# Kernel optimization log

Measured on AMD Instinct MI355X. Metric: run time of the kernel, lower is better.

The kernel has to match this reference:

```python
import jax, jax.numpy as jnp
import numpy as np

B, T, OBS, S, OUT, H = 128, 2048, 128, 128, 64, 64
SCALE = 0.05  # keep the linear recurrence numerically stable over T steps


def setup_inputs() -> dict:
    key = jax.random.key(0)
    ks = jax.random.split(key, 8)
    return {
        "obs": jax.random.normal(ks[0], (B, T, OBS), dtype=jnp.float32),
        "x0": jnp.zeros((B, S), dtype=jnp.float32),
        "A_T": SCALE * jax.random.normal(ks[1], (S, S), dtype=jnp.float32),
        "By_T": SCALE * jax.random.normal(ks[2], (OBS, S), dtype=jnp.float32),
        "Cu_T": SCALE * jax.random.normal(ks[3], (S, OUT), dtype=jnp.float32),
        "Duy_T": SCALE * jax.random.normal(ks[4], (OBS, OUT), dtype=jnp.float32),
        "log_stds": jnp.full((OUT,), -1.6094379124341003, dtype=jnp.float32),
        "W0": SCALE * jax.random.normal(ks[5], (H, OBS), dtype=jnp.float32),
        "b0": jnp.zeros((H,), dtype=jnp.float32),
        "W1": SCALE * jax.random.normal(ks[6], (H, H), dtype=jnp.float32),
        "b1": jnp.zeros((H,), dtype=jnp.float32),
        "W2": SCALE * jax.random.normal(ks[7], (1, H), dtype=jnp.float32),
        "b2": jnp.zeros((1,), dtype=jnp.float32),
        "dt": jnp.float32(0.01),
    }


def reference(obs, x0, A_T, By_T, Cu_T, Duy_T, log_stds, W0, b0, W1, b1, W2, b2, dt):
    def xdot(x, y):
        return x @ A_T + y @ By_T

    def step(x, y):
        # control output at current state, then RK4 integration of x' = A x + B y
        u = x @ Cu_T + y @ Duy_T                      # [B, OUT]
        k1 = xdot(x, y)
        k2 = xdot(x + dt * k1 / 2, y)
        k3 = xdot(x + dt * k2 / 2, y)
        k4 = xdot(x + dt * k3, y)
        x_next = x + dt / 6 * (k1 + 2 * k2 + 2 * k3 + k4)
        return x_next, u

    obs_t = jnp.swapaxes(obs, 0, 1)                   # [T, B, OBS]
    x_final, actions_t = jax.lax.scan(step, x0, obs_t)
    actions = jnp.swapaxes(actions_t, 0, 1)           # [B, T, OUT]

    logs = jnp.broadcast_to(log_stds, (actions.shape[0], actions.shape[1], log_stds.shape[0]))
    outputs = jnp.concatenate([actions, logs], axis=2)  # [B, T, 2*OUT]

    # value MLP: Linear -> tanh -> Linear -> tanh -> Linear
    h = jnp.tanh(obs @ W0.T + b0)
    h = jnp.tanh(h @ W1.T + b1)
    cur_value = (h @ W2.T + b2).reshape(-1)           # [B*T]

    return outputs, cur_value, x_final
```

## Files before the change

### kernel.cpp

```cpp
#include <hip/hip_runtime.h>

#define B_    128
#define T_    2048
#define OBS_  128
#define S_    128
#define OUT_  64
#define H_    64
#define NR    (B_*T_)
#define K_CH  32
#define C_CH  64
#define VOFF  (NR*2*OUT_)
#define XFOFF (VOFF + NR)

typedef __attribute__((ext_vector_type(8))) short short8v;
typedef __attribute__((ext_vector_type(4))) float f32x4;

__device__ __forceinline__ unsigned short f2bf(float f){
  unsigned int u = __float_as_uint(f);
  u += 0x7FFFu + ((u >> 16) & 1u);
  return (unsigned short)(u >> 16);
}
__device__ __forceinline__ float bf2f(unsigned short h){
  return __uint_as_float(((unsigned int)h) << 16);
}

__global__ __launch_bounds__(256) void k_mm(const float* __restrict__ A,
                                            const float* __restrict__ B,
                                            float* __restrict__ C, int ldc){
  int e = blockIdx.x * 256 + threadIdx.x;
  int r = e >> 7, c = e & 127;
  float acc = 0.f;
  #pragma unroll 4
  for (int k = 0; k < 128; ++k) acc += A[r*128 + k] * B[k*128 + c];
  C[r*ldc + c] = acc;
}

__global__ __launch_bounds__(256) void k_build(const float* __restrict__ A_T,
                                               const float* __restrict__ A2,
                                               const float* __restrict__ A3,
                                               const float* __restrict__ A4,
                                               const float* __restrict__ Cu_T,
                                               const float* __restrict__ Duy_T,
                                               const float* __restrict__ dtp,
                                               float* __restrict__ M,
                                               unsigned short* __restrict__ Mmibf,
                                               float* __restrict__ P, float* __restrict__ Wcat,
                                               unsigned short* __restrict__ cubf){
  float dt = *dtp;
  float d2 = dt*dt*0.5f;
  float d3 = d2*dt*(1.f/3.f);
  float d4 = d3*dt*0.25f;
  int e = blockIdx.x * 256 + threadIdx.x;
  int r = e >> 7, c = e & 127;
  float eye = (r == c) ? 1.f : 0.f;
  float mi = dt*A_T[e] + d2*A2[e] + d3*A3[e] + d4*A4[e];
  M[e] = eye + mi;
  Mmibf[e] = f2bf(mi);
  P[e] = dt*eye + d2*A_T[e] + d3*A2[e] + d4*A3[e];
  if (e < 128*64){
    int k = e >> 6, o = e & 63;
    Wcat[k*192 + 128 + o] = Duy_T[e];
    cubf[e] = f2bf(Cu_T[e]);
  }
}

__global__ __launch_bounds__(256) void k_cvtw(const float* __restrict__ Wcat,
                                              const float* __restrict__ W0,
                                              const float* __restrict__ W1,
                                              unsigned short* __restrict__ Wbf,
                                              unsigned short* __restrict__ W0bf,
                                              unsigned short* __restrict__ W1bf){
  int e = blockIdx.x * 256 + threadIdx.x;
  if (e < 24576)       Wbf[e]          = f2bf(Wcat[e]);
  else if (e < 32768)  W0bf[e - 24576] = f2bf(W0[e - 24576]);
  else                 W1bf[e - 32768] = f2bf(W1[e - 32768]);
}

__global__ __launch_bounds__(256) void k_fused(const float* __restrict__ obs,
                                               const unsigned short* __restrict__ Wbf,
                                               const unsigned short* __restrict__ W0bf,
                                               const unsigned short* __restrict__ W1bf,
                                               const float* __restrict__ W2,
                                               const float* __restrict__ b0g,
                                               const float* __restrict__ b1g,
                                               const float* __restrict__ b2g,
                                               const float* __restrict__ ls,
                                               unsigned short* __restrict__ cuy,
                                               float* __restrict__ out){
  __shared__ __align__(16) unsigned short ct[128*200];
  __shared__ __align__(16) unsigned short h0l[128*80];
  __shared__ float pl[128][4];
  int tid = threadIdx.x;
  int lane = tid & 63, w = tid >> 6;
  size_t row0 = (size_t)blockIdx.x * 128;
  int colbase = w * 48;
  int colh    = w * 16;
  int lr = lane & 15;
  int lk = (lane >> 4) * 8;

  short8v bfrag[3][4];
  #pragma unroll
  for (int cf = 0; cf < 3; ++cf)
    #pragma unroll
    for (int kk = 0; kk < 4; ++kk){
      short8v b;
      #pragma unroll
      for (int j = 0; j < 8; ++j)
        b[j] = (short)Wbf[(size_t)(kk*32 + lk + j)*192 + (colbase + cf*16 + lr)];
      bfrag[cf][kk] = b;
    }
  short8v bw0[4];
  #pragma unroll
  for (int kk = 0; kk < 4; ++kk)
    bw0[kk] = *(const short8v*)&W0bf[(size_t)(colh + lr)*128 + kk*32 + lk];
  short8v bw1[2];
  #pragma unroll
  for (int kk = 0; kk < 2; ++kk)
    bw1[kk] = *(const short8v*)&W1bf[(size_t)(colh + lr)*64 + kk*32 + lk];
  float b0v = b0g[colh + lr];
  float b1v = b1g[colh + lr];
  float w2v = W2[colh + lr];

  for (int rf = 0; rf < 8; ++rf){
    f32x4 acc0 = {0.f,0.f,0.f,0.f}, acc1 = {0.f,0.f,0.f,0.f}, acc2 = {0.f,0.f,0.f,0.f};
    f32x4 acch = {0.f,0.f,0.f,0.f};
    const float* arow = obs + (row0 + (size_t)(rf*16 + lr)) * 128;
    #pragma unroll
    for (int kk = 0; kk < 4; ++kk){
      float4 a0 = *(const float4*)&arow[kk*32 + lk];
      float4 a1 = *(const float4*)&arow[kk*32 + lk + 4];
      short8v af;
      af[0] = (short)f2bf(a0.x); af[1] = (short)f2bf(a0.y);
      af[2] = (short)f2bf(a0.z); af[3] = (short)f2bf(a0.w);
      af[4] = (short)f2bf(a1.x); af[5] = (short)f2bf(a1.y);
      af[6] = (short)f2bf(a1.z); af[7] = (short)f2bf(a1.w);
      acc0 = __builtin_amdgcn_mfma_f32_16x16x32_bf16(af, bfrag[0][kk], acc0, 0, 0, 0);
      acc1 = __builtin_amdgcn_mfma_f32_16x16x32_bf16(af, bfrag[1][kk], acc1, 0, 0, 0);
      acc2 = __builtin_amdgcn_mfma_f32_16x16x32_bf16(af, bfrag[2][kk], acc2, 0, 0, 0);
      acch = __builtin_amdgcn_mfma_f32_16x16x32_bf16(af, bw0[kk],     acch, 0, 0, 0);
    }
    int orow = rf*16 + (lane >> 4)*4;
    #pragma unroll
    for (int j = 0; j < 4; ++j){
      ct[(orow + j)*200 + colbase      + lr] = f2bf(acc0[j]);
      ct[(orow + j)*200 + colbase + 16 + lr] = f2bf(acc1[j]);
      ct[(orow + j)*200 + colbase + 32 + lr] = f2bf(acc2[j]);
      h0l[(orow + j)*80 + colh + lr]         = f2bf(tanhf(acch[j] + b0v));
    }
  }
  __syncthreads();

  for (int li = tid; li < 128*24; li += 256){
    int r = li / 24, seg = li % 24;
    *(uint4*)&cuy[(row0 + r)*192 + seg*8] = *(const uint4*)&ct[r*200 + seg*8];
  }

  for (int rf = 0; rf < 8; ++rf){
    f32x4 acc = {b1v, b1v, b1v, b1v};
    #pragma unroll
    for (int kk = 0; kk < 2; ++kk){
      short8v af = *(const short8v*)&h0l[(rf*16 + lr)*80 + kk*32 + lk];
      acc = __builtin_amdgcn_mfma_f32_16x16x32_bf16(af, bw1[kk], acc, 0, 0, 0);
    }
    float4 vpart;
    #pragma unroll
    for (int j = 0; j < 4; ++j) (&vpart.x)[j] = tanhf(acc[j]) * w2v;
    #pragma unroll
    for (int m = 1; m < 16; m <<= 1){
      vpart.x += __shfl_xor(vpart.x, m);
      vpart.y += __shfl_xor(vpart.y, m);
      vpart.z += __shfl_xor(vpart.z, m);
      vpart.w += __shfl_xor(vpart.w, m);
    }
    if (lr == 0){
      int orow = rf*16 + (lane >> 4)*4;
      #pragma unroll
      for (int j = 0; j < 4; ++j) pl[orow + j][w] = (&vpart.x)[j];
    }
  }
  __syncthreads();

  if (tid < 128)
    out[(size_t)VOFF + row0 + tid] = pl[tid][0] + pl[tid][1] + pl[tid][2] + pl[tid][3] + b2g[0];
  for (int li = tid; li < 128*16; li += 256){
    int r = li >> 4, c4 = li & 15;
    float4 lv = *(const float4*)&ls[c4*4];
    *(float4*)&out[(row0 + r)*128 + 64 + c4*4] = lv;
  }
}

__global__ __launch_bounds__(256) void k_phase1(const unsigned short* __restrict__ cuy,
                                                const unsigned short* __restrict__ Mmibf,
                                                float* __restrict__ Dd){
  __shared__ __align__(16) unsigned short xw[32*136];
  int tid = threadIdx.x;
  int lane = tid & 63, w = tid >> 6;
  int lr = lane & 15, lg = lane >> 4;
  int ci = blockIdx.x >> 2, bi = blockIdx.x & 3;
  int b0 = bi*32, t0 = ci*K_CH;
  int colbase = w*32;

  short8v bm[2][4];
  #pragma unroll
  for (int ctt = 0; ctt < 2; ++ctt)
    #pragma unroll
    for (int kk = 0; kk < 4; ++kk){
      short8v b;
      #pragma unroll
      for (int j = 0; j < 8; ++j)
        b[j] = (short)Mmibf[(size_t)(kk*32 + lg*8 + j)*128 + colbase + ctt*16 + lr];
      bm[ctt][kk] = b;
    }

  f32x4 acc[2][2];
  #pragma unroll
  for (int rt = 0; rt < 2; ++rt)
    #pragma unroll
    for (int ctt = 0; ctt < 2; ++ctt)
      #pragma unroll
      for (int j = 0; j < 4; ++j)
        acc[rt][ctt][j] = bf2f(cuy[((size_t)(b0 + rt*16 + lg*4 + j)*T_ + t0)*192 + colbase + ctt*16 + lr]);

  for (int s = 1; s < K_CH; ++s){
    unsigned short cn[2][2][4];
    #pragma unroll
    for (int rt = 0; rt < 2; ++rt)
      #pragma unroll
      for (int ctt = 0; ctt < 2; ++ctt)
        #pragma unroll
        for (int j = 0; j < 4; ++j)
          cn[rt][ctt][j] = cuy[((size_t)(b0 + rt*16 + lg*4 + j)*T_ + t0 + s)*192 + colbase + ctt*16 + lr];
    #pragma unroll
    for (int rt = 0; rt < 2; ++rt)
      #pragma unroll
      for (int ctt = 0; ctt < 2; ++ctt)
        #pragma unroll
        for (int j = 0; j < 4; ++j)
          xw[(rt*16 + lg*4 + j)*136 + colbase + ctt*16 + lr] = f2bf(acc[rt][ctt][j]);
    __syncthreads();
    short8v af[2][4];
    #pragma unroll
    for (int rt = 0; rt < 2; ++rt)
      #pragma unroll
      for (int kk = 0; kk < 4; ++kk)
        af[rt][kk] = *(const short8v*)&xw[(rt*16 + lr)*136 + kk*32 + lg*8];
    __syncthreads();
    #pragma unroll
    for (int rt = 0; rt < 2; ++rt)
      #pragma unroll
      for (int ctt = 0; ctt < 2; ++ctt)
        #pragma unroll
        for (int kk = 0; kk < 4; ++kk)
          acc[rt][ctt] = __builtin_amdgcn_mfma_f32_16x16x32_bf16(af[rt][kk], bm[ctt][kk], acc[rt][ctt], 0, 0, 0);
    #pragma unroll
    for (int rt = 0; rt < 2; ++rt)
      #pragma unroll
      for (int ctt = 0; ctt < 2; ++ctt)
        #pragma unroll
        for (int j = 0; j < 4; ++j)
          acc[rt][ctt][j] += bf2f(cn[rt][ctt][j]);
  }
  #pragma unroll
  for (int rt = 0; rt < 2; ++rt)
    #pragma unroll
    for (int ctt = 0; ctt < 2; ++ctt)
      #pragma unroll
      for (int j = 0; j < 4; ++j)
        Dd[(size_t)ci*16384 + (size_t)(b0 + rt*16 + lg*4 + j)*128 + colbase + ctt*16 + lr] = acc[rt][ctt][j];
}

__global__ __launch_bounds__(256) void k_combine(const float* __restrict__ Mk,
                                                 const float* __restrict__ Dd,
                                                 const float* __restrict__ x0,
                                                 float* __restrict__ XS,
                                                 float* __restrict__ xfin){
  __shared__ float xl[128];
  __shared__ float pl[256];
  int tid = threadIdx.x;
  int b = blockIdx.x;
  int c = tid & 127, h = tid >> 7;
  float mreg[64];
  #pragma unroll
  for (int j = 0; j < 64; ++j) mreg[j] = Mk[(64*h + j)*128 + c];
  if (tid < 128) xl[tid] = x0[(size_t)b*128 + tid];
  __syncthreads();
  for (int i = 0; i < C_CH; ++i){
    if (tid < 128) XS[(size_t)i*16384 + (size_t)b*128 + tid] = xl[tid];
    float part = 0.f;
    #pragma unroll
    for (int jj = 0; jj < 64; jj += 4){
      float4 xv = *(const float4*)&xl[64*h + jj];
      part += xv.x*mreg[jj] + xv.y*mreg[jj+1] + xv.z*mreg[jj+2] + xv.w*mreg[jj+3];
    }
    pl[tid] = part;
    __syncthreads();
    if (tid < 128)
      xl[tid] = pl[tid] + pl[tid + 128] + Dd[(size_t)i*16384 + (size_t)b*128 + tid];
    __syncthreads();
  }
  if (tid < 128) xfin[(size_t)b*128 + tid] = xl[tid];
}

__global__ __launch_bounds__(256) void k_phase3(const unsigned short* __restrict__ cuy,
                                                const unsigned short* __restrict__ Mmibf,
                                                const unsigned short* __restrict__ cubf,
                                                const float* __restrict__ XS,
                                                float* __restrict__ out){
  __shared__ __align__(16) unsigned short xw[32*136];
  int tid = threadIdx.x;
  int lane = tid & 63, w = tid >> 6;
  int lr = lane & 15, lg = lane >> 4;
  int ci = blockIdx.x >> 2, bi = blockIdx.x & 3;
  int b0 = bi*32, t0 = ci*K_CH;
  int colbase = w*32;
  int ucolbase = w*16;

  short8v bm[2][4];
  #pragma unroll
  for (int ctt = 0; ctt < 2; ++ctt)
    #pragma unroll
    for (int kk = 0; kk < 4; ++kk){
      short8v b;
      #pragma unroll
      for (int j = 0; j < 8; ++j)
        b[j] = (short)Mmibf[(size_t)(kk*32 + lg*8 + j)*128 + colbase + ctt*16 + lr];
      bm[ctt][kk] = b;
    }
  short8v bc[4];
  #pragma unroll
  for (int kk = 0; kk < 4; ++kk){
    short8v b;
    #pragma unroll
    for (int j = 0; j < 8; ++j)
      b[j] = (short)cubf[(size_t)(kk*32 + lg*8 + j)*64 + ucolbase + lr];
    bc[kk] = b;
  }

  f32x4 acc[2][2];
  #pragma unroll
  for (int rt = 0; rt < 2; ++rt)
    #pragma unroll
    for (int ctt = 0; ctt < 2; ++ctt)
      #pragma unroll
      for (int j = 0; j < 4; ++j)
        acc[rt][ctt][j] = XS[(size_t)ci*16384 + (size_t)(b0 + rt*16 + lg*4 + j)*128 + colbase + ctt*16 + lr];

  for (int s = 0; s < K_CH; ++s){
    f32x4 au[2];
    #pragma unroll
    for (int rt = 0; rt < 2; ++rt)
      #pragma unroll
      for (int j = 0; j < 4; ++j)
        au[rt][j] = bf2f(cuy[((size_t)(b0 + rt*16 + lg*4 + j)*T_ + t0 + s)*192 + 128 + ucolbase + lr]);
    unsigned short cn[2][2][4];
    if (s + 1 < K_CH){
      #pragma unroll
      for (int rt = 0; rt < 2; ++rt)
        #pragma unroll
        for (int ctt = 0; ctt < 2; ++ctt)
          #pragma unroll
          for (int j = 0; j < 4; ++j)
            cn[rt][ctt][j] = cuy[((size_t)(b0 + rt*16 + lg*4 + j)*T_ + t0 + s)*192 + colbase + ctt*16 + lr];
    }
    #pragma unroll
    for (int rt = 0; rt < 2; ++rt)
      #pragma unroll
      for (int ctt = 0; ctt < 2; ++ctt)
        #pragma unroll
        for (int j = 0; j < 4; ++j)
          xw[(rt*16 + lg*4 + j)*136 + colbase + ctt*16 + lr] = f2bf(acc[rt][ctt][j]);
    __syncthreads();
    short8v af[2][4];
    #pragma unroll
    for (int rt = 0; rt < 2; ++rt)
      #pragma unroll
      for (int kk = 0; kk < 4; ++kk)
        af[rt][kk] = *(const short8v*)&xw[(rt*16 + lr)*136 + kk*32 + lg*8];
    __syncthreads();
    #pragma unroll
    for (int rt = 0; rt < 2; ++rt)
      #pragma unroll
      for (int kk = 0; kk < 4; ++kk)
        au[rt] = __builtin_amdgcn_mfma_f32_16x16x32_bf16(af[rt][kk], bc[kk], au[rt], 0, 0, 0);
    #pragma unroll
    for (int rt = 0; rt < 2; ++rt)
      #pragma unroll
      for (int j = 0; j < 4; ++j)
        out[((size_t)(b0 + rt*16 + lg*4 + j)*T_ + t0 + s)*128 + ucolbase + lr] = au[rt][j];
    if (s + 1 < K_CH){
      #pragma unroll
      for (int rt = 0; rt < 2; ++rt)
        #pragma unroll
        for (int ctt = 0; ctt < 2; ++ctt)
          #pragma unroll
          for (int kk = 0; kk < 4; ++kk)
            acc[rt][ctt] = __builtin_amdgcn_mfma_f32_16x16x32_bf16(af[rt][kk], bm[ctt][kk], acc[rt][ctt], 0, 0, 0);
      #pragma unroll
      for (int rt = 0; rt < 2; ++rt)
        #pragma unroll
        for (int ctt = 0; ctt < 2; ++ctt)
          #pragma unroll
          for (int j = 0; j < 4; ++j)
            acc[rt][ctt][j] += bf2f(cn[rt][ctt][j]);
    }
  }
}

extern "C" void kernel_launch(void* const* d_in, const int* in_sizes, int n_in,
                              void* d_out, int out_size, void* d_ws, size_t ws_size,
                              hipStream_t stream){
  const float* obs  = (const float*)d_in[0];
  const float* x0   = (const float*)d_in[1];
  const float* A_T  = (const float*)d_in[2];
  const float* By_T = (const float*)d_in[3];
  const float* Cu_T = (const float*)d_in[4];
  const float* Duy_T= (const float*)d_in[5];
  const float* ls   = (const float*)d_in[6];
  const float* W0   = (const float*)d_in[7];
  const float* b0   = (const float*)d_in[8];
  const float* W1   = (const float*)d_in[9];
  const float* b1   = (const float*)d_in[10];
  const float* W2   = (const float*)d_in[11];
  const float* b2   = (const float*)d_in[12];
  const float* dt   = (const float*)d_in[13];
  float* out = (float*)d_out;

  char* ws = (char*)d_ws;
  unsigned short* cuy = (unsigned short*)(ws + 0);
  float* A2     = (float*)(ws + 100663296);
  float* A3     = (float*)(ws + 100728832);
  float* A4     = (float*)(ws + 100794368);
  float* Mm     = (float*)(ws + 100859904);
  float* Pp     = (float*)(ws + 100925440);
  float* Mk     = (float*)(ws + 100990976);
  float* sq1    = (float*)(ws + 101056512);
  float* sq2    = (float*)(ws + 101122048);
  unsigned short* Mmibf = (unsigned short*)(ws + 101187584);
  float* Wcat   = (float*)(ws + 101255168);
  unsigned short* cubf  = (unsigned short*)(ws + 101353472);
  float* Dd     = (float*)(ws + 101387264);
  float* XS     = (float*)(ws + 105581568);
  unsigned short* Wbf  = (unsigned short*)Pp;
  unsigned short* W0bf = (unsigned short*)sq2;
  unsigned short* W1bf = (unsigned short*)(((char*)sq2) + 16384);

  k_mm<<<64, 256, 0, stream>>>(A_T, A_T, A2, 128);
  k_mm<<<64, 256, 0, stream>>>(A2, A_T, A3, 128);
  k_mm<<<64, 256, 0, stream>>>(A2, A2, A4, 128);
  k_build<<<64, 256, 0, stream>>>(A_T, A2, A3, A4, Cu_T, Duy_T, dt, Mm, Mmibf, Pp, Wcat, cubf);
  k_mm<<<64, 256, 0, stream>>>(By_T, Pp, Wcat, 192);
  k_mm<<<64, 256, 0, stream>>>(Mm, Mm, sq1, 128);
  k_mm<<<64, 256, 0, stream>>>(sq1, sq1, sq2, 128);
  k_mm<<<64, 256, 0, stream>>>(sq2, sq2, sq1, 128);
  k_mm<<<64, 256, 0, stream>>>(sq1, sq1, sq2, 128);
  k_mm<<<64, 256, 0, stream>>>(sq2, sq2, Mk, 128);
  k_cvtw<<<144, 256, 0, stream>>>(Wcat, W0, W1, Wbf, W0bf, W1bf);

  k_fused<<<NR/128, 256, 0, stream>>>(obs, Wbf, W0bf, W1bf, W2, b0, b1, b2, ls, cuy, out);
  k_phase1<<<C_CH*4, 256, 0, stream>>>(cuy, Mmibf, Dd);
  k_combine<<<B_, 256, 0, stream>>>(Mk, Dd, x0, XS, out + XFOFF);
  k_phase3<<<C_CH*4, 256, 0, stream>>>(cuy, Mmibf, cubf, XS, out);
}
```

Baseline: 319.5 us.

## Fuse setup matmuls into one cooperative kernel, halve chunk length, shrink LDS

Eleven small setup launches (matrix powers, builds, weight conversions) become one cooperative kernel that uses grid syncs between stages, which cuts launch overhead. The chunked scan moves from 64 chunks of 32 steps to 128 chunks of 16 steps, giving phase kernels more blocks and shorter serial loops but a longer combine. The fused kernel now stages its output in two halves, halving the ct LDS buffer, which may raise occupancy. Software bf16 rounding is replaced by the HIP intrinsics, including a packed pair conversion. The risks are that all cooperative blocks must be co-resident, that the Dd buffer doubles in size, and that the combine kernel gets more serial work.

```diff
diff --git a/kernel.cpp b/kernel.cpp
--- a/kernel.cpp
+++ b/kernel.cpp
@@ -1,4 +1,6 @@
 #include <hip/hip_runtime.h>
+#include <hip/hip_bf16.h>
+#include <hip/hip_cooperative_groups.h>
 
 #define B_    128
 #define T_    2048
@@ -7,73 +9,100 @@
 #define OUT_  64
 #define H_    64
 #define NR    (B_*T_)
-#define K_CH  32
-#define C_CH  64
+#define K_CH  16
+#define C_CH  128
 #define VOFF  (NR*2*OUT_)
 #define XFOFF (VOFF + NR)
 
 typedef __attribute__((ext_vector_type(8))) short short8v;
 typedef __attribute__((ext_vector_type(4))) float f32x4;
 
-__device__ __forceinline__ unsigned short f2bf(float f){
-  unsigned int u = __float_as_uint(f);
-  u += 0x7FFFu + ((u >> 16) & 1u);
-  return (unsigned short)(u >> 16);
+__device__ __forceinline__ unsigned short f2bf_hw(float f){
+  __hip_bfloat16 h = __float2bfloat16(f);
+  union { __hip_bfloat16 hh; unsigned short u; } cv; cv.hh = h; return cv.u;
+}
+__device__ __forceinline__ unsigned int pk2(float a, float b){
+  __hip_bfloat162 h = __float22bfloat162_rn(make_float2(a, b));
+  union { __hip_bfloat162 h2; unsigned int u; } cv; cv.h2 = h; return cv.u;
 }
 __device__ __forceinline__ float bf2f(unsigned short h){
   return __uint_as_float(((unsigned int)h) << 16);
 }
 
-__global__ __launch_bounds__(256) void k_mm(const float* __restrict__ A,
-                                            const float* __restrict__ B,
-                                            float* __restrict__ C, int ldc){
-  int e = blockIdx.x * 256 + threadIdx.x;
-  int r = e >> 7, c = e & 127;
-  float acc = 0.f;
-  #pragma unroll 4
-  for (int k = 0; k < 128; ++k) acc += A[r*128 + k] * B[k*128 + c];
-  C[r*ldc + c] = acc;
-}
-
-__global__ __launch_bounds__(256) void k_build(const float* __restrict__ A_T,
-                                               const float* __restrict__ A2,
-                                               const float* __restrict__ A3,
-                                               const float* __restrict__ A4,
+__global__ __launch_bounds__(256) void k_setup(const float* __restrict__ A_T,
+                                               const float* __restrict__ By_T,
                                                const float* __restrict__ Cu_T,
                                                const float* __restrict__ Duy_T,
                                                const float* __restrict__ dtp,
-                                               float* __restrict__ M,
+                                               const float* __restrict__ W0,
+                                               const float* __restrict__ W1,
+                                               float* __restrict__ A2, float* __restrict__ A3,
+                                               float* __restrict__ A4, float* __restrict__ Mm,
+                                               float* __restrict__ Pp, float* __restrict__ Mk,
+                                               float* __restrict__ sq1, float* __restrict__ sq2,
                                                unsigned short* __restrict__ Mmibf,
-                                               float* __restrict__ P, float* __restrict__ Wcat,
-                                               unsigned short* __restrict__ cubf){
-  float dt = *dtp;
-  float d2 = dt*dt*0.5f;
-  float d3 = d2*dt*(1.f/3.f);
-  float d4 = d3*dt*0.25f;
-  int e = blockIdx.x * 256 + threadIdx.x;
-  int r = e >> 7, c = e & 127;
-  float eye = (r == c) ? 1.f : 0.f;
-  float mi = dt*A_T[e] + d2*A2[e] + d3*A3[e] + d4*A4[e];
-  M[e] = eye + mi;
-  Mmibf[e] = f2bf(mi);
-  P[e] = dt*eye + d2*A_T[e] + d3*A2[e] + d4*A3[e];
-  if (e < 128*64){
-    int k = e >> 6, o = e & 63;
-    Wcat[k*192 + 128 + o] = Duy_T[e];
-    cubf[e] = f2bf(Cu_T[e]);
-  }
-}
-
-__global__ __launch_bounds__(256) void k_cvtw(const float* __restrict__ Wcat,
-                                              const float* __restrict__ W0,
-                                              const float* __restrict__ W1,
-                                              unsigned short* __restrict__ Wbf,
-                                              unsigned short* __restrict__ W0bf,
-                                              unsigned short* __restrict__ W1bf){
-  int e = blockIdx.x * 256 + threadIdx.x;
-  if (e < 24576)       Wbf[e]          = f2bf(Wcat[e]);
-  else if (e < 32768)  W0bf[e - 24576] = f2bf(W0[e - 24576]);
-  else                 W1bf[e - 32768] = f2bf(W1[e - 32768]);
+                                               float* __restrict__ Wcat,
+                                               unsigned short* __restrict__ cubf,
+                                               unsigned short* __restrict__ Wbf,
+                                               unsigned short* __restrict__ W0bf,
+                                               unsigned short* __restrict__ W1bf){
+  cooperative_groups::grid_group g = cooperative_groups::this_grid();
+  int gid = blockIdx.x * 256 + threadIdx.x;
+  int r = gid >> 7, c = gid & 127;
+  { float a = 0.f;
+    #pragma unroll 4
+    for (int k = 0; k < 128; ++k) a += A_T[r*128+k] * A_T[k*128+c];
+    A2[gid] = a; }
+  g.sync();
+  { float a3 = 0.f, a4 = 0.f;
+    #pragma unroll 4
+    for (int k = 0; k < 128; ++k){
+      float l = A2[r*128+k];
+      a3 += l * A_T[k*128+c];
+      a4 += l * A2[k*128+c];
+    }
+    A3[gid] = a3; A4[gid] = a4; }
+  g.sync();
+  { float dt = *dtp;
+    float d2 = dt*dt*0.5f;
+    float d3 = d2*dt*(1.f/3.f);
+    float d4 = d3*dt*0.25f;
+    float eye = (r == c) ? 1.f : 0.f;
+    float mi = dt*A_T[gid] + d2*A2[gid] + d3*A3[gid] + d4*A4[gid];
+    Mm[gid] = eye + mi;
+    Mmibf[gid] = f2bf_hw(mi);
+    Pp[gid] = dt*eye + d2*A_T[gid] + d3*A2[gid] + d4*A3[gid];
+    if (gid < 128*64){
+      int k = gid >> 6, o = gid & 63;
+      Wcat[k*192 + 128 + o] = Duy_T[gid];
+      cubf[gid] = f2bf_hw(Cu_T[gid]);
+    } }
+  g.sync();
+  { float ga = 0.f, m2 = 0.f;
+    #pragma unroll 4
+    for (int k = 0; k < 128; ++k){
+      ga += By_T[r*128+k] * Pp[k*128+c];
+      m2 += Mm[r*128+k] * Mm[k*128+c];
+    }
+    Wcat[r*192 + c] = ga; sq1[gid] = m2; }
+  g.sync();
+  { float m4 = 0.f;
+    #pragma unroll 4
+    for (int k = 0; k < 128; ++k) m4 += sq1[r*128+k] * sq1[k*128+c];
+    sq2[gid] = m4;
+    for (int e = gid; e < 24576; e += 16384) Wbf[e] = f2bf_hw(Wcat[e]);
+    if (gid < 8192) W0bf[gid] = f2bf_hw(W0[gid]);
+    if (gid < 4096) W1bf[gid] = f2bf_hw(W1[gid]); }
+  g.sync();
+  { float m8 = 0.f;
+    #pragma unroll 4
+    for (int k = 0; k < 128; ++k) m8 += sq2[r*128+k] * sq2[k*128+c];
+    sq1[gid] = m8; }
+  g.sync();
+  { float m16 = 0.f;
+    #pragma unroll 4
+    for (int k = 0; k < 128; ++k) m16 += sq1[r*128+k] * sq1[k*128+c];
+    Mk[gid] = m16; }
 }
 
 __global__ __launch_bounds__(256) void k_fused(const float* __restrict__ obs,
@@ -87,7 +116,7 @@
                                                const float* __restrict__ ls,
                                                unsigned short* __restrict__ cuy,
                                                float* __restrict__ out){
-  __shared__ __align__(16) unsigned short ct[128*200];
+  __shared__ __align__(16) unsigned short ct[64*200];
   __shared__ __align__(16) unsigned short h0l[128*80];
   __shared__ float pl[128][4];
   int tid = threadIdx.x;
@@ -121,38 +150,40 @@
   float b1v = b1g[colh + lr];
   float w2v = W2[colh + lr];
 
-  for (int rf = 0; rf < 8; ++rf){
-    f32x4 acc0 = {0.f,0.f,0.f,0.f}, acc1 = {0.f,0.f,0.f,0.f}, acc2 = {0.f,0.f,0.f,0.f};
-    f32x4 acch = {0.f,0.f,0.f,0.f};
-    const float* arow = obs + (row0 + (size_t)(rf*16 + lr)) * 128;
-    #pragma unroll
-    for (int kk = 0; kk < 4; ++kk){
-      float4 a0 = *(const float4*)&arow[kk*32 + lk];
-      float4 a1 = *(const float4*)&arow[kk*32 + lk + 4];
-      short8v af;
-      af[0] = (short)f2bf(a0.x); af[1] = (short)f2bf(a0.y);
-      af[2] = (short)f2bf(a0.z); af[3] = (short)f2bf(a0.w);
-      af[4] = (short)f2bf(a1.x); af[5] = (short)f2bf(a1.y);
-      af[6] = (short)f2bf(a1.z); af[7] = (short)f2bf(a1.w);
-      acc0 = __builtin_amdgcn_mfma_f32_16x16x32_bf16(af, bfrag[0][kk], acc0, 0, 0, 0);
-      acc1 = __builtin_amdgcn_mfma_f32_16x16x32_bf16(af, bfrag[1][kk], acc1, 0, 0, 0);
-      acc2 = __builtin_amdgcn_mfma_f32_16x16x32_bf16(af, bfrag[2][kk], acc2, 0, 0, 0);
-      acch = __builtin_amdgcn_mfma_f32_16x16x32_bf16(af, bw0[kk],     acch, 0, 0, 0);
-    }
-    int orow = rf*16 + (lane >> 4)*4;
-    #pragma unroll
-    for (int j = 0; j < 4; ++j){
-      ct[(orow + j)*200 + colbase      + lr] = f2bf(acc0[j]);
-      ct[(orow + j)*200 + colbase + 16 + lr] = f2bf(acc1[j]);
-      ct[(orow + j)*200 + colbase + 32 + lr] = f2bf(acc2[j]);
-      h0l[(orow + j)*80 + colh + lr]         = f2bf(tanhf(acch[j] + b0v));
-    }
-  }
-  __syncthreads();
-
-  for (int li = tid; li < 128*24; li += 256){
-    int r = li / 24, seg = li % 24;
-    *(uint4*)&cuy[(row0 + r)*192 + seg*8] = *(const uint4*)&ct[r*200 + seg*8];
+  for (int h = 0; h < 2; ++h){
+    for (int rf = 4*h; rf < 4*h + 4; ++rf){
+      f32x4 acc0 = {0.f,0.f,0.f,0.f}, acc1 = {0.f,0.f,0.f,0.f}, acc2 = {0.f,0.f,0.f,0.f};
+      f32x4 acch = {0.f,0.f,0.f,0.f};
+      const float* arow = obs + (row0 + (size_t)(rf*16 + lr)) * 128;
+      #pragma unroll
+      for (int kk = 0; kk < 4; ++kk){
+        float4 a0 = *(const float4*)&arow[kk*32 + lk];
+        float4 a1 = *(const float4*)&arow[kk*32 + lk + 4];
+        union { unsigned int u[4]; short8v v; } afu;
+        afu.u[0] = pk2(a0.x, a0.y); afu.u[1] = pk2(a0.z, a0.w);
+        afu.u[2] = pk2(a1.x, a1.y); afu.u[3] = pk2(a1.z, a1.w);
+        short8v af = afu.v;
+        acc0 = __builtin_amdgcn_mfma_f32_16x16x32_bf16(af, bfrag[0][kk], acc0, 0, 0, 0);
+        acc1 = __builtin_amdgcn_mfma_f32_16x16x32_bf16(af, bfrag[1][kk], acc1, 0, 0, 0);
+        acc2 = __builtin_amdgcn_mfma_f32_16x16x32_bf16(af, bfrag[2][kk], acc2, 0, 0, 0);
+        acch = __builtin_amdgcn_mfma_f32_16x16x32_bf16(af, bw0[kk],     acch, 0, 0, 0);
+      }
+      int orow = rf*16 + (lane >> 4)*4;
+      int crow = (rf - 4*h)*16 + (lane >> 4)*4;
+      #pragma unroll
+      for (int j = 0; j < 4; ++j){
+        ct[(crow + j)*200 + colbase      + lr] = f2bf_hw(acc0[j]);
+        ct[(crow + j)*200 + colbase + 16 + lr] = f2bf_hw(acc1[j]);
+        ct[(crow + j)*200 + colbase + 32 + lr] = f2bf_hw(acc2[j]);
+        h0l[(orow + j)*80 + colh + lr]         = f2bf_hw(tanhf(acch[j] + b0v));
+      }
+    }
+    __syncthreads();
+    for (int li = tid; li < 64*24; li += 256){
+      int r = li / 24, seg = li % 24;
+      *(uint4*)&cuy[(row0 + 64*h + r)*192 + seg*8] = *(const uint4*)&ct[r*200 + seg*8];
+    }
+    __syncthreads();
   }
 
   for (int rf = 0; rf < 8; ++rf){
@@ -236,7 +267,7 @@
       for (int ctt = 0; ctt < 2; ++ctt)
         #pragma unroll
         for (int j = 0; j < 4; ++j)
-          xw[(rt*16 + lg*4 + j)*136 + colbase + ctt*16 + lr] = f2bf(acc[rt][ctt][j]);
+          xw[(rt*16 + lg*4 + j)*136 + colbase + ctt*16 + lr] = f2bf_hw(acc[rt][ctt][j]);
     __syncthreads();
     short8v af[2][4];
     #pragma unroll
@@ -368,7 +399,7 @@
       for (int ctt = 0; ctt < 2; ++ctt)
         #pragma unroll
         for (int j = 0; j < 4; ++j)
-          xw[(rt*16 + lg*4 + j)*136 + colbase + ctt*16 + lr] = f2bf(acc[rt][ctt][j]);
+          xw[(rt*16 + lg*4 + j)*136 + colbase + ctt*16 + lr] = f2bf_hw(acc[rt][ctt][j]);
     __syncthreads();
     short8v af[2][4];
     #pragma unroll
@@ -439,22 +470,19 @@
   float* Wcat   = (float*)(ws + 101255168);
   unsigned short* cubf  = (unsigned short*)(ws + 101353472);
   float* Dd     = (float*)(ws + 101387264);
-  float* XS     = (float*)(ws + 105581568);
+  float* XS     = (float*)(ws + 109775872);
   unsigned short* Wbf  = (unsigned short*)Pp;
-  unsigned short* W0bf = (unsigned short*)sq2;
-  unsigned short* W1bf = (unsigned short*)(((char*)sq2) + 16384);
-
-  k_mm<<<64, 256, 0, stream>>>(A_T, A_T, A2, 128);
-  k_mm<<<64, 256, 0, stream>>>(A2, A_T, A3, 128);
-  k_mm<<<64, 256, 0, stream>>>(A2, A2, A4, 128);
-  k_build<<<64, 256, 0, stream>>>(A_T, A2, A3, A4, Cu_T, Duy_T, dt, Mm, Mmibf, Pp, Wcat, cubf);
-  k_mm<<<64, 256, 0, stream>>>(By_T, Pp, Wcat, 192);
-  k_mm<<<64, 256, 0, stream>>>(Mm, Mm, sq1, 128);
-  k_mm<<<64, 256, 0, stream>>>(sq1, sq1, sq2, 128);
-  k_mm<<<64, 256, 0, stream>>>(sq2, sq2, sq1, 128);
-  k_mm<<<64, 256, 0, stream>>>(sq1, sq1, sq2, 128);
-  k_mm<<<64, 256, 0, stream>>>(sq2, sq2, Mk, 128);
-  k_cvtw<<<144, 256, 0, stream>>>(Wcat, W0, W1, Wbf, W0bf, W1bf);
+  unsigned short* W0bf = (unsigned short*)A3;
+  unsigned short* W1bf = (unsigned short*)A4;
+
+  void* args[] = {
+    (void*)&A_T, (void*)&By_T, (void*)&Cu_T, (void*)&Duy_T, (void*)&dt,
+    (void*)&W0, (void*)&W1,
+    (void*)&A2, (void*)&A3, (void*)&A4, (void*)&Mm, (void*)&Pp, (void*)&Mk,
+    (void*)&sq1, (void*)&sq2, (void*)&Mmibf, (void*)&Wcat, (void*)&cubf,
+    (void*)&Wbf, (void*)&W0bf, (void*)&W1bf
+  };
+  hipLaunchCooperativeKernel((void*)k_setup, dim3(64), dim3(256), args, 0, stream);
 
   k_fused<<<NR/128, 256, 0, stream>>>(obs, Wbf, W0bf, W1bf, W2, b0, b1, b2, ls, cuy, out);
   k_phase1<<<C_CH*4, 256, 0, stream>>>(cuy, Mmibf, Dd);
```

After: 378.5 us. 18.5% more time.

## Fuse setup matmul kernels, use hardware bf16 conversion, stage obs tile in LDS

Applied to the files above, without the earlier changes.

Merges several small 128x128 setup matmul launches into combined kernels (A3/A4 together, By*P with M^2, M^4 with weight conversion), cutting the launch count from twelve to eight. Replaces the software round-to-nearest bf16 conversion with the HIP bf16 intrinsics. In k_fused, obs rows are converted to bf16 once and staged in LDS in 64-row halves with coalesced loads. The output staging buffer shrinks to 16 rows and is flushed after every row fragment, which lowers LDS use but adds two barriers per fragment.

```diff
diff --git a/kernel.cpp b/kernel.cpp
--- a/kernel.cpp
+++ b/kernel.cpp
@@ -1,4 +1,5 @@
 #include <hip/hip_runtime.h>
+#include <hip/hip_bf16.h>
 
 #define B_    128
 #define T_    2048
@@ -15,10 +16,13 @@
 typedef __attribute__((ext_vector_type(8))) short short8v;
 typedef __attribute__((ext_vector_type(4))) float f32x4;
 
-__device__ __forceinline__ unsigned short f2bf(float f){
-  unsigned int u = __float_as_uint(f);
-  u += 0x7FFFu + ((u >> 16) & 1u);
-  return (unsigned short)(u >> 16);
+__device__ __forceinline__ unsigned short f2bf_hw(float f){
+  __hip_bfloat16 h = __float2bfloat16(f);
+  union { __hip_bfloat16 hh; unsigned short u; } cv; cv.hh = h; return cv.u;
+}
+__device__ __forceinline__ unsigned int pk2(float a, float b){
+  __hip_bfloat162 h = __float22bfloat162_rn(make_float2(a, b));
+  union { __hip_bfloat162 h2; unsigned int u; } cv; cv.h2 = h; return cv.u;
 }
 __device__ __forceinline__ float bf2f(unsigned short h){
   return __uint_as_float(((unsigned int)h) << 16);
@@ -33,6 +37,22 @@
   #pragma unroll 4
   for (int k = 0; k < 128; ++k) acc += A[r*128 + k] * B[k*128 + c];
   C[r*ldc + c] = acc;
+}
+
+__global__ __launch_bounds__(256) void k_mm2(const float* __restrict__ A_T,
+                                             const float* __restrict__ A2,
+                                             float* __restrict__ A3,
+                                             float* __restrict__ A4){
+  int e = blockIdx.x * 256 + threadIdx.x;
+  int r = e >> 7, c = e & 127;
+  float a3 = 0.f, a4 = 0.f;
+  #pragma unroll 4
+  for (int k = 0; k < 128; ++k){
+    float l = A2[r*128 + k];
+    a3 += l * A_T[k*128 + c];
+    a4 += l * A2[k*128 + c];
+  }
+  A3[e] = a3; A4[e] = a4;
 }
 
 __global__ __launch_bounds__(256) void k_build(const float* __restrict__ A_T,
@@ -55,25 +75,49 @@
   float eye = (r == c) ? 1.f : 0.f;
   float mi = dt*A_T[e] + d2*A2[e] + d3*A3[e] + d4*A4[e];
   M[e] = eye + mi;
-  Mmibf[e] = f2bf(mi);
+  Mmibf[e] = f2bf_hw(mi);
   P[e] = dt*eye + d2*A_T[e] + d3*A2[e] + d4*A3[e];
   if (e < 128*64){
     int k = e >> 6, o = e & 63;
     Wcat[k*192 + 128 + o] = Duy_T[e];
-    cubf[e] = f2bf(Cu_T[e]);
-  }
-}
-
-__global__ __launch_bounds__(256) void k_cvtw(const float* __restrict__ Wcat,
-                                              const float* __restrict__ W0,
-                                              const float* __restrict__ W1,
-                                              unsigned short* __restrict__ Wbf,
-                                              unsigned short* __restrict__ W0bf,
-                                              unsigned short* __restrict__ W1bf){
+    cubf[e] = f2bf_hw(Cu_T[e]);
+  }
+}
+
+__global__ __launch_bounds__(256) void k_gm2(const float* __restrict__ By_T,
+                                             const float* __restrict__ Pp,
+                                             const float* __restrict__ Mm,
+                                             float* __restrict__ Wcat,
+                                             float* __restrict__ sq1){
   int e = blockIdx.x * 256 + threadIdx.x;
-  if (e < 24576)       Wbf[e]          = f2bf(Wcat[e]);
-  else if (e < 32768)  W0bf[e - 24576] = f2bf(W0[e - 24576]);
-  else                 W1bf[e - 32768] = f2bf(W1[e - 32768]);
+  int r = e >> 7, c = e & 127;
+  float ga = 0.f, m2 = 0.f;
+  #pragma unroll 4
+  for (int k = 0; k < 128; ++k){
+    ga += By_T[r*128 + k] * Pp[k*128 + c];
+    m2 += Mm[r*128 + k] * Mm[k*128 + c];
+  }
+  Wcat[r*192 + c] = ga;
+  sq1[e] = m2;
+}
+
+__global__ __launch_bounds__(256) void k_m4cvt(const float* __restrict__ sq1,
+                                               const float* __restrict__ Wcat,
+                                               const float* __restrict__ W0,
+                                               const float* __restrict__ W1,
+                                               float* __restrict__ sq2,
+                                               unsigned short* __restrict__ Wbf,
+                                               unsigned short* __restrict__ W0bf,
+                                               unsigned short* __restrict__ W1bf){
+  int e = blockIdx.x * 256 + threadIdx.x;
+  int r = e >> 7, c = e & 127;
+  float m4 = 0.f;
+  #pragma unroll 4
+  for (int k = 0; k < 128; ++k) m4 += sq1[r*128 + k] * sq1[k*128 + c];
+  sq2[e] = m4;
+  for (int i = e; i < 24576; i += 16384) Wbf[i] = f2bf_hw(Wcat[i]);
+  if (e < 8192) W0bf[e] = f2bf_hw(W0[e]);
+  if (e < 4096) W1bf[e] = f2bf_hw(W1[e]);
 }
 
 __global__ __launch_bounds__(256) void k_fused(const float* __restrict__ obs,
@@ -87,7 +131,8 @@
                                                const float* __restrict__ ls,
                                                unsigned short* __restrict__ cuy,
                                                float* __restrict__ out){
-  __shared__ __align__(16) unsigned short ct[128*200];
+  __shared__ __align__(16) unsigned short ylds[64*136];
+  __shared__ __align__(16) unsigned short ct[16*200];
   __shared__ __align__(16) unsigned short h0l[128*80];
   __shared__ float pl[128][4];
   int tid = threadIdx.x;
@@ -121,38 +166,50 @@
   float b1v = b1g[colh + lr];
   float w2v = W2[colh + lr];
 
-  for (int rf = 0; rf < 8; ++rf){
-    f32x4 acc0 = {0.f,0.f,0.f,0.f}, acc1 = {0.f,0.f,0.f,0.f}, acc2 = {0.f,0.f,0.f,0.f};
-    f32x4 acch = {0.f,0.f,0.f,0.f};
-    const float* arow = obs + (row0 + (size_t)(rf*16 + lr)) * 128;
-    #pragma unroll
-    for (int kk = 0; kk < 4; ++kk){
-      float4 a0 = *(const float4*)&arow[kk*32 + lk];
-      float4 a1 = *(const float4*)&arow[kk*32 + lk + 4];
-      short8v af;
-      af[0] = (short)f2bf(a0.x); af[1] = (short)f2bf(a0.y);
-      af[2] = (short)f2bf(a0.z); af[3] = (short)f2bf(a0.w);
-      af[4] = (short)f2bf(a1.x); af[5] = (short)f2bf(a1.y);
-      af[6] = (short)f2bf(a1.z); af[7] = (short)f2bf(a1.w);
-      acc0 = __builtin_amdgcn_mfma_f32_16x16x32_bf16(af, bfrag[0][kk], acc0, 0, 0, 0);
-      acc1 = __builtin_amdgcn_mfma_f32_16x16x32_bf16(af, bfrag[1][kk], acc1, 0, 0, 0);
-      acc2 = __builtin_amdgcn_mfma_f32_16x16x32_bf16(af, bfrag[2][kk], acc2, 0, 0, 0);
-      acch = __builtin_amdgcn_mfma_f32_16x16x32_bf16(af, bw0[kk],     acch, 0, 0, 0);
-    }
-    int orow = rf*16 + (lane >> 4)*4;
-    #pragma unroll
-    for (int j = 0; j < 4; ++j){
-      ct[(orow + j)*200 + colbase      + lr] = f2bf(acc0[j]);
-      ct[(orow + j)*200 + colbase + 16 + lr] = f2bf(acc1[j]);
-      ct[(orow + j)*200 + colbase + 32 + lr] = f2bf(acc2[j]);
-      h0l[(orow + j)*80 + colh + lr]         = f2bf(tanhf(acch[j] + b0v));
-    }
-  }
-  __syncthreads();
-
-  for (int li = tid; li < 128*24; li += 256){
-    int r = li / 24, seg = li % 24;
-    *(uint4*)&cuy[(row0 + r)*192 + seg*8] = *(const uint4*)&ct[r*200 + seg*8];
+  for (int h = 0; h < 2; ++h){
+    {
+      int base = tid * 32;
+      int r = base >> 7, c0 = base & 127;
+      const float* grow = obs + (row0 + h*64 + r) * 128;
+      #pragma unroll
+      for (int it = 0; it < 4; ++it){
+        float4 a0 = *(const float4*)&grow[c0 + it*8];
+        float4 a1 = *(const float4*)&grow[c0 + it*8 + 4];
+        uint4 pv;
+        pv.x = pk2(a0.x, a0.y); pv.y = pk2(a0.z, a0.w);
+        pv.z = pk2(a1.x, a1.y); pv.w = pk2(a1.z, a1.w);
+        *(uint4*)&ylds[r*136 + c0 + it*8] = pv;
+      }
+    }
+    __syncthreads();
+    for (int rfh = 0; rfh < 4; ++rfh){
+      int rf = h*4 + rfh;
+      f32x4 acc0 = {0.f,0.f,0.f,0.f}, acc1 = {0.f,0.f,0.f,0.f}, acc2 = {0.f,0.f,0.f,0.f};
+      f32x4 acch = {0.f,0.f,0.f,0.f};
+      #pragma unroll
+      for (int kk = 0; kk < 4; ++kk){
+        short8v af = *(const short8v*)&ylds[(rfh*16 + lr)*136 + kk*32 + lk];
+        acc0 = __builtin_amdgcn_mfma_f32_16x16x32_bf16(af, bfrag[0][kk], acc0, 0, 0, 0);
+        acc1 = __builtin_amdgcn_mfma_f32_16x16x32_bf16(af, bfrag[1][kk], acc1, 0, 0, 0);
+        acc2 = __builtin_amdgcn_mfma_f32_16x16x32_bf16(af, bfrag[2][kk], acc2, 0, 0, 0);
+        acch = __builtin_amdgcn_mfma_f32_16x16x32_bf16(af, bw0[kk],     acch, 0, 0, 0);
+      }
+      int orow = rf*16 + (lane >> 4)*4;
+      int crow = (lane >> 4)*4;
+      #pragma unroll
+      for (int j = 0; j < 4; ++j){
+        ct[(crow + j)*200 + colbase      + lr] = f2bf_hw(acc0[j]);
+        ct[(crow + j)*200 + colbase + 16 + lr] = f2bf_hw(acc1[j]);
+        ct[(crow + j)*200 + colbase + 32 + lr] = f2bf_hw(acc2[j]);
+        h0l[(orow + j)*80 + colh + lr]         = f2bf_hw(tanhf(acch[j] + b0v));
+      }
+      __syncthreads();
+      for (int li = tid; li < 16*24; li += 256){
+        int r = li / 24, seg = li % 24;
+        *(uint4*)&cuy[(row0 + h*64 + rfh*16 + r)*192 + seg*8] = *(const uint4*)&ct[r*200 + seg*8];
+      }
+      __syncthreads();
+    }
   }
 
   for (int rf = 0; rf < 8; ++rf){
@@ -236,7 +293,7 @@
       for (int ctt = 0; ctt < 2; ++ctt)
         #pragma unroll
         for (int j = 0; j < 4; ++j)
-          xw[(rt*16 + lg*4 + j)*136 + colbase + ctt*16 + lr] = f2bf(acc[rt][ctt][j]);
+          xw[(rt*16 + lg*4 + j)*136 + colbase + ctt*16 + lr] = f2bf_hw(acc[rt][ctt][j]);
     __syncthreads();
     short8v af[2][4];
     #pragma unroll
@@ -368,7 +425,7 @@
       for (int ctt = 0; ctt < 2; ++ctt)
         #pragma unroll
         for (int j = 0; j < 4; ++j)
-          xw[(rt*16 + lg*4 + j)*136 + colbase + ctt*16 + lr] = f2bf(acc[rt][ctt][j]);
+          xw[(rt*16 + lg*4 + j)*136 + colbase + ctt*16 + lr] = f2bf_hw(acc[rt][ctt][j]);
     __syncthreads();
     short8v af[2][4];
     #pragma unroll
@@ -441,20 +498,17 @@
   float* Dd     = (float*)(ws + 101387264);
   float* XS     = (float*)(ws + 105581568);
   unsigned short* Wbf  = (unsigned short*)Pp;
-  unsigned short* W0bf = (unsigned short*)sq2;
-  unsigned short* W1bf = (unsigned short*)(((char*)sq2) + 16384);
-
-  k_mm<<<64, 256, 0, stream>>>(A_T, A_T, A2, 128);
-  k_mm<<<64, 256, 0, stream>>>(A2, A_T, A3, 128);
-  k_mm<<<64, 256, 0, stream>>>(A2, A2, A4, 128);
+  unsigned short* W0bf = (unsigned short*)A3;
+  unsigned short* W1bf = (unsigned short*)A4;
+
+  k_mm   <<<64, 256, 0, stream>>>(A_T, A_T, A2, 128);
+  k_mm2  <<<64, 256, 0, stream>>>(A_T, A2, A3, A4);
   k_build<<<64, 256, 0, stream>>>(A_T, A2, A3, A4, Cu_T, Duy_T, dt, Mm, Mmibf, Pp, Wcat, cubf);
-  k_mm<<<64, 256, 0, stream>>>(By_T, Pp, Wcat, 192);
-  k_mm<<<64, 256, 0, stream>>>(Mm, Mm, sq1, 128);
-  k_mm<<<64, 256, 0, stream>>>(sq1, sq1, sq2, 128);
-  k_mm<<<64, 256, 0, stream>>>(sq2, sq2, sq1, 128);
-  k_mm<<<64, 256, 0, stream>>>(sq1, sq1, sq2, 128);
-  k_mm<<<64, 256, 0, stream>>>(sq2, sq2, Mk, 128);
-  k_cvtw<<<144, 256, 0, stream>>>(Wcat, W0, W1, Wbf, W0bf, W1bf);
+  k_gm2  <<<64, 256, 0, stream>>>(By_T, Pp, Mm, Wcat, sq1);
+  k_m4cvt<<<64, 256, 0, stream>>>(sq1, Wcat, W0, W1, sq2, Wbf, W0bf, W1bf);
+  k_mm   <<<64, 256, 0, stream>>>(sq2, sq2, sq1, 128);
+  k_mm   <<<64, 256, 0, stream>>>(sq1, sq1, sq2, 128);
+  k_mm   <<<64, 256, 0, stream>>>(sq2, sq2, Mk, 128);
 
   k_fused<<<NR/128, 256, 0, stream>>>(obs, Wbf, W0bf, W1bf, W2, b0, b1, b2, ls, cuy, out);
   k_phase1<<<C_CH*4, 256, 0, stream>>>(cuy, Mmibf, Dd);
```

New measurement: 278.4 us. -12.9%, faster.
